# Optimization experiments

Measured on AMD Instinct MI355X. Metric: run time of the kernel, lower is better.

The kernel has to match this reference:

```python
import jax, jax.numpy as jnp
import numpy as np

N_HEADS = 16
D_MODEL = 1024
D_KV = 64


def setup_inputs() -> dict:
    key = jax.random.key(0)
    ks = jax.random.split(key, 5)
    x = jax.random.normal(ks[0], (4, 2048, D_MODEL), dtype=jnp.float32)
    # per-head projections stacked: [H, D_MODEL, D_KV]
    WQ = jax.random.normal(ks[1], (N_HEADS, D_MODEL, D_KV), dtype=jnp.float32) * (D_MODEL ** -0.5)
    WK = jax.random.normal(ks[2], (N_HEADS, D_MODEL, D_KV), dtype=jnp.float32) * (D_MODEL ** -0.5)
    WV = jax.random.normal(ks[3], (N_HEADS, D_MODEL, D_KV), dtype=jnp.float32) * (D_MODEL ** -0.5)
    WO = jax.random.normal(ks[4], (N_HEADS * D_KV, D_MODEL), dtype=jnp.float32) * ((N_HEADS * D_KV) ** -0.5)
    return {"x": x, "WQ": WQ, "WK": WK, "WV": WV, "WO": WO}


def reference(x, WQ, WK, WV, WO):
    # Batched over heads instead of the original per-head Python loop.
    # q,k,v: [B, H, S, Dk]
    q = jnp.einsum('bsd,hdk->bhsk', x, WQ)
    k = jnp.einsum('bsd,hdk->bhsk', x, WK)
    v = jnp.einsum('bsd,hdk->bhsk', x, WV)
    scale = 1.0 / jnp.sqrt(jnp.asarray(q.shape[-1], q.dtype))
    scores = jnp.einsum('bhqk,bhsk->bhqs', q, k) * scale  # [B, H, S, S]
    attn = jax.nn.softmax(scores, axis=-1)
    o = jnp.einsum('bhqs,bhsk->bhqk', attn, v)            # [B, H, S, Dk]
    # concat heads along feature dim == transpose + reshape
    B, H, S, Dk = o.shape
    o = o.transpose(0, 2, 1, 3).reshape(B, S, H * Dk)
    return o @ WO
```

## Files before the change

kernel.cpp:

```cpp
#include <hip/hip_runtime.h>
#include <stdint.h>
#include <stddef.h>


typedef __attribute__((ext_vector_type(8))) short short8;
typedef __attribute__((ext_vector_type(4))) float floatx4;
typedef __attribute__((ext_vector_type(16))) float floatx16;

#define MFMA_BF16(a, b, c) __builtin_amdgcn_mfma_f32_16x16x32_bf16((a), (b), (c), 0, 0, 0)
#define MFMA32_BF16(a, b, c) __builtin_amdgcn_mfma_f32_32x32x16_bf16((a), (b), (c), 0, 0, 0)

__device__ __forceinline__ unsigned short f32_bf16(float f) {
  union { float f; unsigned u; } v; v.f = f;
  unsigned r = v.u + 0x7fffu + ((v.u >> 16) & 1u);
  return (unsigned short)(r >> 16);
}

__device__ __forceinline__ unsigned pack_bf16_rh(float a, float b) {
  unsigned ua = __float_as_uint(a) + 0x8000u;
  unsigned ub = __float_as_uint(b) + 0x8000u;
  return __builtin_amdgcn_perm(ub, ua, 0x07060302u);
}

__device__ __forceinline__ float fast_exp2(float x) {
#if __has_builtin(__builtin_amdgcn_exp2f)
  return __builtin_amdgcn_exp2f(x);
#else
  return exp2f(x);
#endif
}

__device__ __forceinline__ void g2l16(const void* g, void* l) {
  __builtin_amdgcn_global_load_lds((const __attribute__((address_space(1))) void*)g,
                                   (__attribute__((address_space(3))) void*)l,
                                   16, 0, 0);
}


__global__ __launch_bounds__(256) void cvt_x_k(const float* __restrict__ x,
                                               unsigned short* __restrict__ xb) {
  int i = (blockIdx.x * 256 + threadIdx.x) * 4;
  float4 v = *(const float4*)(x + i);
  ushort4 o;
  o.x = f32_bf16(v.x); o.y = f32_bf16(v.y); o.z = f32_bf16(v.z); o.w = f32_bf16(v.w);
  *(ushort4*)(xb + i) = o;
}

__global__ __launch_bounds__(256) void cvt_wqkv_t(const float* __restrict__ WQ,
                                                  const float* __restrict__ WK,
                                                  const float* __restrict__ WV,
                                                  unsigned short* __restrict__ Wt) {
  __shared__ unsigned short tile[64][72];
  const int th = blockIdx.y;
  const int typ = th >> 4, h = th & 15;
  const float* W = (typ == 0) ? WQ : ((typ == 1) ? WK : WV);
  const float* src = W + ((size_t)h * 1024 + blockIdx.x * 64) * 64;
  const int tid = threadIdx.x;
  #pragma unroll
  for (int it = 0; it < 16; ++it) {
    int f = it * 256 + tid;
    int dk = f & 63, dl = f >> 6;
    tile[dk][dl] = f32_bf16(src[(size_t)dl * 64 + dk]);
  }
  __syncthreads();
  unsigned short* dst = Wt + (size_t)(typ * 1024 + h * 64) * 1024 + blockIdx.x * 64;
  #pragma unroll
  for (int it = 0; it < 16; ++it) {
    int f = it * 256 + tid;
    int d = f & 63, dk = f >> 6;
    dst[(size_t)dk * 1024 + d] = tile[dk][d];
  }
}

__global__ __launch_bounds__(256) void cvt_wo_t(const float* __restrict__ WO,
                                                unsigned short* __restrict__ Wt) {
  __shared__ unsigned short tile[64][72];
  const int nt = blockIdx.x * 64, kt = blockIdx.y * 64;
  const int tid = threadIdx.x;
  #pragma unroll
  for (int it = 0; it < 16; ++it) {
    int f = it * 256 + tid;
    int n = f & 63, kl = f >> 6;
    tile[n][kl] = f32_bf16(WO[(size_t)(kt + kl) * 1024 + nt + n]);
  }
  __syncthreads();
  #pragma unroll
  for (int it = 0; it < 16; ++it) {
    int f = it * 256 + tid;
    int k = f & 63, nl = f >> 6;
    Wt[(size_t)(nt + nl) * 1024 + kt + k] = tile[nl][k];
  }
}


__global__ __launch_bounds__(256, 2)
void gemm_qkv_k(const unsigned short* __restrict__ A,
                const unsigned short* __restrict__ Bt,
                unsigned short* __restrict__ Qo,
                unsigned short* __restrict__ Ko,
                unsigned short* __restrict__ Vo) {
  __shared__ __align__(16) unsigned short As[8192];
  __shared__ __align__(16) unsigned short Bs[8192];
  const int lane = threadIdx.x & 63;
  const int wave = threadIdx.x >> 6;
  const int quad = lane >> 4;
  const int t = lane & 15;
  const int wm = wave >> 1, wn = wave & 1;
  const int row0 = blockIdx.y * 128;
  const int col0 = blockIdx.x * 128;

  floatx4 acc[4][4];
  #pragma unroll
  for (int i = 0; i < 4; ++i)
    #pragma unroll
    for (int j = 0; j < 4; ++j) acc[i][j] = (floatx4)0.0f;

  for (int k0 = 0; k0 < 1024; k0 += 64) {
    #pragma unroll
    for (int i = 0; i < 4; ++i) {
      int s = (wave * 4 + i) * 64 + lane;
      int r = s >> 3, kc = (s & 7) ^ (r & 7);
      g2l16(A  + (size_t)(row0 + r) * 1024 + k0 + kc * 8, As + (wave * 4 + i) * 512);
      g2l16(Bt + (size_t)(col0 + r) * 1024 + k0 + kc * 8, Bs + (wave * 4 + i) * 512);
    }
    __syncthreads();
    #pragma unroll
    for (int kk = 0; kk < 2; ++kk) {
      short8 af[4], bf[4];
      #pragma unroll
      for (int mt = 0; mt < 4; ++mt) {
        int r = wm * 64 + mt * 16 + t;
        int kc = (kk * 4 + quad) ^ (r & 7);
        af[mt] = *(const short8*)(As + (r * 8 + kc) * 8);
      }
      #pragma unroll
      for (int nt = 0; nt < 4; ++nt) {
        int r = wn * 64 + nt * 16 + t;
        int kc = (kk * 4 + quad) ^ (r & 7);
        bf[nt] = *(const short8*)(Bs + (r * 8 + kc) * 8);
      }
      #pragma unroll
      for (int mt = 0; mt < 4; ++mt)
        #pragma unroll
        for (int nt = 0; nt < 4; ++nt)
          acc[mt][nt] = MFMA_BF16(af[mt], bf[nt], acc[mt][nt]);
    }
    __syncthreads();
  }

  const int typ = col0 >> 10;
  const float qscale = 0.18033688011112042f;
  const int qp = ((quad & 1) << 1) | (quad >> 1);
  #pragma unroll
  for (int mt = 0; mt < 4; ++mt) {
    int grow0 = row0 + wm * 64 + mt * 16 + quad * 4;
    int b = grow0 >> 11;
    int s = grow0 & 2047;
    #pragma unroll
    for (int nt = 0; nt < 4; ++nt) {
      int gcol = col0 + wn * 64 + nt * 16 + t;
      int rem = gcol & 1023;
      int h = rem >> 6, dk = rem & 63;
      int bhh = b * 16 + h;
      if (typ == 0) {
        #pragma unroll
        for (int rg = 0; rg < 4; ++rg)
          Qo[((size_t)bhh * 2048 + s + rg) * 64 + dk] = f32_bf16(acc[mt][nt][rg] * qscale);
      } else if (typ == 1) {
        #pragma unroll
        for (int rg = 0; rg < 4; ++rg)
          Ko[((size_t)bhh * 2048 + s + rg) * 64 + dk] = f32_bf16(acc[mt][nt][rg]);
      } else {
        ushort4 pv;
        pv.x = f32_bf16(acc[mt][nt][0]);
        pv.y = f32_bf16(acc[mt][nt][1]);
        pv.z = f32_bf16(acc[mt][nt][2]);
        pv.w = f32_bf16(acc[mt][nt][3]);
        int sp = (s & ~15) | (qp << 2);
        *(ushort4*)(Vo + ((size_t)bhh * 64 + dk) * 2048 + sp) = pv;
      }
    }
  }
}


__global__ __launch_bounds__(256, 4)
void attn_k(const unsigned short* __restrict__ Qg_,
            const unsigned short* __restrict__ Kg_,
            const unsigned short* __restrict__ Vg_,
            unsigned short* __restrict__ O) {
  __shared__ __align__(16) char smem[16384];
  const int lane = threadIdx.x & 63;
  const int wave = threadIdx.x >> 6;
  const int h32 = lane >> 5;
  const int c32 = lane & 31;
  const int bh = blockIdx.y;
  const int q0 = blockIdx.x * 128;
  const unsigned short* Qg = Qg_ + ((size_t)bh * 2048 + q0) * 64;
  const unsigned short* Kg = Kg_ + (size_t)bh * 2048 * 64;
  const unsigned short* Vg = Vg_ + (size_t)bh * 64 * 2048;

  short8 qf[4];
  {
    int rq = wave * 32 + c32;
    #pragma unroll
    for (int dc = 0; dc < 4; ++dc)
      qf[dc] = *(const short8*)(Qg + (size_t)rq * 64 + dc * 16 + h32 * 8);
  }

  union { unsigned u[4]; short8 s8; } onesf;
  #pragma unroll
  for (int i = 0; i < 4; ++i) onesf.u[i] = 0x3F803F80u;

  floatx16 acc[2], accs;
  acc[0] = (floatx16)0.0f; acc[1] = (floatx16)0.0f; accs = (floatx16)0.0f;

  for (int s0 = 0; s0 < 2048; s0 += 64) {
    #pragma unroll
    for (int i = 0; i < 2; ++i) {
      int s = (wave * 2 + i) * 64 + lane;
      int r = s >> 3, kc = (s & 7) ^ (r & 7);
      g2l16(Kg + (size_t)(s0 + r) * 64 + kc * 8, smem + (wave * 2 + i) * 1024);
      g2l16(Vg + (size_t)r * 2048 + s0 + kc * 8, smem + 8192 + (wave * 2 + i) * 1024);
    }
    __syncthreads();

    #pragma unroll
    for (int kb = 0; kb < 2; ++kb) {
      floatx16 sc = (floatx16)0.0f;
      #pragma unroll
      for (int dc = 0; dc < 4; ++dc) {
        int rk = kb * 32 + c32;
        int kc = (dc * 2 + h32) ^ (c32 & 7);
        short8 kf = *(const short8*)(smem + (rk * 8 + kc) * 16);
        sc = MFMA32_BF16(kf, qf[dc], sc);
      }
      float p[16];
      #pragma unroll
      for (int r = 0; r < 16; ++r) p[r] = fast_exp2(sc[r]);
      unsigned pk[8];
      #pragma unroll
      for (int i = 0; i < 8; ++i) pk[i] = pack_bf16_rh(p[2 * i], p[2 * i + 1]);
      union { unsigned u[4]; short8 s8; } a0, a1;
      a0.u[0] = pk[0]; a0.u[1] = pk[1]; a0.u[2] = pk[2]; a0.u[3] = pk[3];
      a1.u[0] = pk[4]; a1.u[1] = pk[5]; a1.u[2] = pk[6]; a1.u[3] = pk[7];
      #pragma unroll
      for (int st = 0; st < 2; ++st) {
        short8 af = st ? a1.s8 : a0.s8;
        int cc = kb * 4 + st * 2 + h32;
        #pragma unroll
        for (int nb = 0; nb < 2; ++nb) {
          int rv = nb * 32 + c32;
          short8 bv = *(const short8*)(smem + 8192 + (rv * 8 + (cc ^ (rv & 7))) * 16);
          acc[nb] = MFMA32_BF16(af, bv, acc[nb]);
        }
        accs = MFMA32_BF16(af, onesf.s8, accs);
      }
    }
    __syncthreads();
  }

  const int b = bh >> 4, h = bh & 15;
  #pragma unroll
  for (int g = 0; g < 4; ++g) {
    #pragma unroll
    for (int rr = 0; rr < 4; ++rr) {
      int qrel = rr + 8 * g + 4 * h32;
      float rl = 1.0f / accs[4 * g + rr];
      int token = b * 2048 + q0 + wave * 32 + qrel;
      size_t base = (size_t)token * 1024 + h * 64;
      O[base + c32]      = f32_bf16(acc[0][4 * g + rr] * rl);
      O[base + 32 + c32] = f32_bf16(acc[1][4 * g + rr] * rl);
    }
  }
}


__global__ __launch_bounds__(256, 2)
void gemm_out_k(const unsigned short* __restrict__ A,
                const unsigned short* __restrict__ Bt,
                float* __restrict__ C) {
  __shared__ __align__(16) unsigned short As[8192];
  __shared__ __align__(16) unsigned short Bs[8192];
  const int lane = threadIdx.x & 63;
  const int wave = threadIdx.x >> 6;
  const int quad = lane >> 4;
  const int t = lane & 15;
  const int wm = wave >> 1, wn = wave & 1;
  const int row0 = blockIdx.y * 128;
  const int col0 = blockIdx.x * 128;

  floatx4 acc[4][4];
  #pragma unroll
  for (int i = 0; i < 4; ++i)
    #pragma unroll
    for (int j = 0; j < 4; ++j) acc[i][j] = (floatx4)0.0f;

  for (int k0 = 0; k0 < 1024; k0 += 64) {
    #pragma unroll
    for (int i = 0; i < 4; ++i) {
      int s = (wave * 4 + i) * 64 + lane;
      int r = s >> 3, kc = (s & 7) ^ (r & 7);
      g2l16(A  + (size_t)(row0 + r) * 1024 + k0 + kc * 8, As + (wave * 4 + i) * 512);
      g2l16(Bt + (size_t)(col0 + r) * 1024 + k0 + kc * 8, Bs + (wave * 4 + i) * 512);
    }
    __syncthreads();
    #pragma unroll
    for (int kk = 0; kk < 2; ++kk) {
      short8 af[4], bf[4];
      #pragma unroll
      for (int mt = 0; mt < 4; ++mt) {
        int r = wm * 64 + mt * 16 + t;
        int kc = (kk * 4 + quad) ^ (r & 7);
        af[mt] = *(const short8*)(As + (r * 8 + kc) * 8);
      }
      #pragma unroll
      for (int nt = 0; nt < 4; ++nt) {
        int r = wn * 64 + nt * 16 + t;
        int kc = (kk * 4 + quad) ^ (r & 7);
        bf[nt] = *(const short8*)(Bs + (r * 8 + kc) * 8);
      }
      #pragma unroll
      for (int mt = 0; mt < 4; ++mt)
        #pragma unroll
        for (int nt = 0; nt < 4; ++nt)
          acc[mt][nt] = MFMA_BF16(af[mt], bf[nt], acc[mt][nt]);
    }
    __syncthreads();
  }

  #pragma unroll
  for (int mt = 0; mt < 4; ++mt) {
    int grow0 = row0 + wm * 64 + mt * 16 + quad * 4;
    #pragma unroll
    for (int nt = 0; nt < 4; ++nt) {
      int gcol = col0 + wn * 64 + nt * 16 + t;
      #pragma unroll
      for (int rg = 0; rg < 4; ++rg)
        C[(size_t)(grow0 + rg) * 1024 + gcol] = acc[mt][nt][rg];
    }
  }
}


extern "C" void kernel_launch(void* const* d_in, const int* in_sizes, int n_in,
                              void* d_out, int out_size, void* d_ws, size_t ws_size,
                              hipStream_t stream) {
  const float* x  = (const float*)d_in[0];
  const float* WQ = (const float*)d_in[1];
  const float* WK = (const float*)d_in[2];
  const float* WV = (const float*)d_in[3];
  const float* WO = (const float*)d_in[4];
  char* ws = (char*)d_ws;
  unsigned short* xb   = (unsigned short*)(ws);
  unsigned short* Wqkv = (unsigned short*)(ws + (size_t)16 * 1024 * 1024);
  unsigned short* WOt  = (unsigned short*)(ws + (size_t)22 * 1024 * 1024);
  unsigned short* Qb   = (unsigned short*)(ws + (size_t)24 * 1024 * 1024);
  unsigned short* Kb   = (unsigned short*)(ws + (size_t)40 * 1024 * 1024);
  unsigned short* Vb   = (unsigned short*)(ws + (size_t)56 * 1024 * 1024);
  float* out = (float*)d_out;

  cvt_x_k<<<8192, 256, 0, stream>>>(x, xb);
  cvt_wqkv_t<<<dim3(16, 48), 256, 0, stream>>>(WQ, WK, WV, Wqkv);
  cvt_wo_t<<<dim3(16, 16), 256, 0, stream>>>(WO, WOt);
  gemm_qkv_k<<<dim3(24, 64), 256, 0, stream>>>(xb, Wqkv, Qb, Kb, Vb);
  attn_k<<<dim3(16, 64), 256, 0, stream>>>(Qb, Kb, Vb, xb );
  gemm_out_k<<<dim3(8, 64), 256, 0, stream>>>(xb, WOt, out);
}
```

Baseline: 261.5 us.

## Double per-wave query rows in attention and merge weight conversion kernels

Each attention wave now processes two 32-row query groups against a shared 128-key K/V tile, so every LDS K/V fragment read feeds two MFMAs and the key loop runs half as many iterations with half as many barriers. The block now covers 256 queries, the grid is reordered so head-batch is the fast dimension, LDS doubles to 32KB and the occupancy hint drops to 2 blocks per CU. The two weight transpose-convert kernels are merged into a single launch. The cost is higher register pressure from the doubled accumulators and fewer resident blocks for hiding latency.

```diff
diff --git a/kernel.cpp b/kernel.cpp
--- a/kernel.cpp
+++ b/kernel.cpp
@@ -46,49 +46,50 @@
   *(ushort4*)(xb + i) = o;
 }
 
-__global__ __launch_bounds__(256) void cvt_wqkv_t(const float* __restrict__ WQ,
-                                                  const float* __restrict__ WK,
-                                                  const float* __restrict__ WV,
-                                                  unsigned short* __restrict__ Wt) {
+__global__ __launch_bounds__(256) void cvt_w_k(const float* __restrict__ WQ,
+                                               const float* __restrict__ WK,
+                                               const float* __restrict__ WV,
+                                               const float* __restrict__ WO,
+                                               unsigned short* __restrict__ Wqkv,
+                                               unsigned short* __restrict__ WOt) {
   __shared__ unsigned short tile[64][72];
-  const int th = blockIdx.y;
-  const int typ = th >> 4, h = th & 15;
-  const float* W = (typ == 0) ? WQ : ((typ == 1) ? WK : WV);
-  const float* src = W + ((size_t)h * 1024 + blockIdx.x * 64) * 64;
+  const int bid = blockIdx.x;
   const int tid = threadIdx.x;
-  #pragma unroll
-  for (int it = 0; it < 16; ++it) {
-    int f = it * 256 + tid;
-    int dk = f & 63, dl = f >> 6;
-    tile[dk][dl] = f32_bf16(src[(size_t)dl * 64 + dk]);
-  }
-  __syncthreads();
-  unsigned short* dst = Wt + (size_t)(typ * 1024 + h * 64) * 1024 + blockIdx.x * 64;
-  #pragma unroll
-  for (int it = 0; it < 16; ++it) {
-    int f = it * 256 + tid;
-    int d = f & 63, dk = f >> 6;
-    dst[(size_t)dk * 1024 + d] = tile[dk][d];
-  }
-}
-
-__global__ __launch_bounds__(256) void cvt_wo_t(const float* __restrict__ WO,
-                                                unsigned short* __restrict__ Wt) {
-  __shared__ unsigned short tile[64][72];
-  const int nt = blockIdx.x * 64, kt = blockIdx.y * 64;
-  const int tid = threadIdx.x;
-  #pragma unroll
-  for (int it = 0; it < 16; ++it) {
-    int f = it * 256 + tid;
-    int n = f & 63, kl = f >> 6;
-    tile[n][kl] = f32_bf16(WO[(size_t)(kt + kl) * 1024 + nt + n]);
-  }
-  __syncthreads();
-  #pragma unroll
-  for (int it = 0; it < 16; ++it) {
-    int f = it * 256 + tid;
-    int k = f & 63, nl = f >> 6;
-    Wt[(size_t)(nt + nl) * 1024 + kt + k] = tile[nl][k];
+  if (bid < 768) {
+    const int th = bid >> 4;
+    const int typ = th >> 4, h = th & 15;
+    const float* W = (typ == 0) ? WQ : ((typ == 1) ? WK : WV);
+    const float* src = W + ((size_t)h * 1024 + (bid & 15) * 64) * 64;
+    #pragma unroll
+    for (int it = 0; it < 16; ++it) {
+      int f = it * 256 + tid;
+      int dk = f & 63, dl = f >> 6;
+      tile[dk][dl] = f32_bf16(src[(size_t)dl * 64 + dk]);
+    }
+    __syncthreads();
+    unsigned short* dst = Wqkv + (size_t)(typ * 1024 + h * 64) * 1024 + (bid & 15) * 64;
+    #pragma unroll
+    for (int it = 0; it < 16; ++it) {
+      int f = it * 256 + tid;
+      int d = f & 63, dk = f >> 6;
+      dst[(size_t)dk * 1024 + d] = tile[dk][d];
+    }
+  } else {
+    const int id2 = bid - 768;
+    const int nt = (id2 & 15) * 64, kt = (id2 >> 4) * 64;
+    #pragma unroll
+    for (int it = 0; it < 16; ++it) {
+      int f = it * 256 + tid;
+      int n = f & 63, kl = f >> 6;
+      tile[n][kl] = f32_bf16(WO[(size_t)(kt + kl) * 1024 + nt + n]);
+    }
+    __syncthreads();
+    #pragma unroll
+    for (int it = 0; it < 16; ++it) {
+      int f = it * 256 + tid;
+      int k = f & 63, nl = f >> 6;
+      WOt[(size_t)(nt + nl) * 1024 + kt + k] = tile[nl][k];
+    }
   }
 }
 
@@ -184,77 +185,86 @@
 }
 
 
-__global__ __launch_bounds__(256, 4)
+__global__ __launch_bounds__(256, 2)
 void attn_k(const unsigned short* __restrict__ Qg_,
             const unsigned short* __restrict__ Kg_,
             const unsigned short* __restrict__ Vg_,
             unsigned short* __restrict__ O) {
-  __shared__ __align__(16) char smem[16384];
+  __shared__ __align__(16) char smem[32768];
   const int lane = threadIdx.x & 63;
   const int wave = threadIdx.x >> 6;
   const int h32 = lane >> 5;
   const int c32 = lane & 31;
-  const int bh = blockIdx.y;
-  const int q0 = blockIdx.x * 128;
+  const int bh = blockIdx.x;
+  const int q0 = blockIdx.y * 256;
   const unsigned short* Qg = Qg_ + ((size_t)bh * 2048 + q0) * 64;
   const unsigned short* Kg = Kg_ + (size_t)bh * 2048 * 64;
   const unsigned short* Vg = Vg_ + (size_t)bh * 64 * 2048;
 
-  short8 qf[4];
-  {
-    int rq = wave * 32 + c32;
+  short8 qf[2][4];
+  #pragma unroll
+  for (int g = 0; g < 2; ++g) {
+    int rq = wave * 64 + g * 32 + c32;
     #pragma unroll
     for (int dc = 0; dc < 4; ++dc)
-      qf[dc] = *(const short8*)(Qg + (size_t)rq * 64 + dc * 16 + h32 * 8);
+      qf[g][dc] = *(const short8*)(Qg + (size_t)rq * 64 + dc * 16 + h32 * 8);
   }
 
   union { unsigned u[4]; short8 s8; } onesf;
   #pragma unroll
   for (int i = 0; i < 4; ++i) onesf.u[i] = 0x3F803F80u;
 
-  floatx16 acc[2], accs;
-  acc[0] = (floatx16)0.0f; acc[1] = (floatx16)0.0f; accs = (floatx16)0.0f;
-
-  for (int s0 = 0; s0 < 2048; s0 += 64) {
-    #pragma unroll
-    for (int i = 0; i < 2; ++i) {
-      int s = (wave * 2 + i) * 64 + lane;
-      int r = s >> 3, kc = (s & 7) ^ (r & 7);
-      g2l16(Kg + (size_t)(s0 + r) * 64 + kc * 8, smem + (wave * 2 + i) * 1024);
-      g2l16(Vg + (size_t)r * 2048 + s0 + kc * 8, smem + 8192 + (wave * 2 + i) * 1024);
-    }
-    __syncthreads();
-
-    #pragma unroll
-    for (int kb = 0; kb < 2; ++kb) {
-      floatx16 sc = (floatx16)0.0f;
+  floatx16 acc[2][2], accs[2];
+  #pragma unroll
+  for (int g = 0; g < 2; ++g) {
+    acc[g][0] = (floatx16)0.0f; acc[g][1] = (floatx16)0.0f; accs[g] = (floatx16)0.0f;
+  }
+
+  for (int s0 = 0; s0 < 2048; s0 += 128) {
+    #pragma unroll
+    for (int i = 0; i < 4; ++i) {
+      int s = (wave * 4 + i) * 64 + lane;
+      int rk = s >> 3, ck = (s & 7) ^ (rk & 7);
+      g2l16(Kg + (size_t)(s0 + rk) * 64 + ck * 8, smem + s * 16);
+      int rv = s >> 4, cv = (s & 15) ^ (rv & 7);
+      g2l16(Vg + (size_t)rv * 2048 + s0 + cv * 8, smem + 16384 + s * 16);
+    }
+    __syncthreads();
+
+    #pragma unroll
+    for (int kb = 0; kb < 4; ++kb) {
+      floatx16 sc0 = (floatx16)0.0f, sc1 = (floatx16)0.0f;
       #pragma unroll
       for (int dc = 0; dc < 4; ++dc) {
         int rk = kb * 32 + c32;
-        int kc = (dc * 2 + h32) ^ (c32 & 7);
+        int kc = (dc * 2 + h32) ^ (rk & 7);
         short8 kf = *(const short8*)(smem + (rk * 8 + kc) * 16);
-        sc = MFMA32_BF16(kf, qf[dc], sc);
-      }
-      float p[16];
-      #pragma unroll
-      for (int r = 0; r < 16; ++r) p[r] = fast_exp2(sc[r]);
-      unsigned pk[8];
-      #pragma unroll
-      for (int i = 0; i < 8; ++i) pk[i] = pack_bf16_rh(p[2 * i], p[2 * i + 1]);
-      union { unsigned u[4]; short8 s8; } a0, a1;
-      a0.u[0] = pk[0]; a0.u[1] = pk[1]; a0.u[2] = pk[2]; a0.u[3] = pk[3];
-      a1.u[0] = pk[4]; a1.u[1] = pk[5]; a1.u[2] = pk[6]; a1.u[3] = pk[7];
+        sc0 = MFMA32_BF16(kf, qf[0][dc], sc0);
+        sc1 = MFMA32_BF16(kf, qf[1][dc], sc1);
+      }
+      unsigned pk0[8], pk1[8];
+      #pragma unroll
+      for (int i = 0; i < 8; ++i) {
+        float a0 = fast_exp2(sc0[2 * i]), b0 = fast_exp2(sc0[2 * i + 1]);
+        float a1 = fast_exp2(sc1[2 * i]), b1 = fast_exp2(sc1[2 * i + 1]);
+        pk0[i] = pack_bf16_rh(a0, b0);
+        pk1[i] = pack_bf16_rh(a1, b1);
+      }
       #pragma unroll
       for (int st = 0; st < 2; ++st) {
-        short8 af = st ? a1.s8 : a0.s8;
+        union { unsigned u[4]; short8 s8; } af0, af1;
+        #pragma unroll
+        for (int i = 0; i < 4; ++i) { af0.u[i] = pk0[4 * st + i]; af1.u[i] = pk1[4 * st + i]; }
         int cc = kb * 4 + st * 2 + h32;
         #pragma unroll
         for (int nb = 0; nb < 2; ++nb) {
           int rv = nb * 32 + c32;
-          short8 bv = *(const short8*)(smem + 8192 + (rv * 8 + (cc ^ (rv & 7))) * 16);
-          acc[nb] = MFMA32_BF16(af, bv, acc[nb]);
+          short8 bv = *(const short8*)(smem + 16384 + (rv * 16 + (cc ^ (rv & 7))) * 16);
+          acc[0][nb] = MFMA32_BF16(af0.s8, bv, acc[0][nb]);
+          acc[1][nb] = MFMA32_BF16(af1.s8, bv, acc[1][nb]);
         }
-        accs = MFMA32_BF16(af, onesf.s8, accs);
+        accs[0] = MFMA32_BF16(af0.s8, onesf.s8, accs[0]);
+        accs[1] = MFMA32_BF16(af1.s8, onesf.s8, accs[1]);
       }
     }
     __syncthreads();
@@ -262,15 +272,18 @@
 
   const int b = bh >> 4, h = bh & 15;
   #pragma unroll
-  for (int g = 0; g < 4; ++g) {
-    #pragma unroll
-    for (int rr = 0; rr < 4; ++rr) {
-      int qrel = rr + 8 * g + 4 * h32;
-      float rl = 1.0f / accs[4 * g + rr];
-      int token = b * 2048 + q0 + wave * 32 + qrel;
-      size_t base = (size_t)token * 1024 + h * 64;
-      O[base + c32]      = f32_bf16(acc[0][4 * g + rr] * rl);
-      O[base + 32 + c32] = f32_bf16(acc[1][4 * g + rr] * rl);
+  for (int g = 0; g < 2; ++g) {
+    #pragma unroll
+    for (int gg = 0; gg < 4; ++gg) {
+      #pragma unroll
+      for (int rr = 0; rr < 4; ++rr) {
+        int qrel = rr + 8 * gg + 4 * h32;
+        float rl = 1.0f / accs[g][4 * gg + rr];
+        int token = b * 2048 + q0 + wave * 64 + g * 32 + qrel;
+        size_t base = (size_t)token * 1024 + h * 64;
+        O[base + c32]      = f32_bf16(acc[g][0][4 * gg + rr] * rl);
+        O[base + 32 + c32] = f32_bf16(acc[g][1][4 * gg + rr] * rl);
+      }
     }
   }
 }
@@ -361,9 +374,8 @@
   float* out = (float*)d_out;
 
   cvt_x_k<<<8192, 256, 0, stream>>>(x, xb);
-  cvt_wqkv_t<<<dim3(16, 48), 256, 0, stream>>>(WQ, WK, WV, Wqkv);
-  cvt_wo_t<<<dim3(16, 16), 256, 0, stream>>>(WO, WOt);
+  cvt_w_k<<<1024, 256, 0, stream>>>(WQ, WK, WV, WO, Wqkv, WOt);
   gemm_qkv_k<<<dim3(24, 64), 256, 0, stream>>>(xb, Wqkv, Qb, Kb, Vb);
-  attn_k<<<dim3(16, 64), 256, 0, stream>>>(Qb, Kb, Vb, xb );
+  attn_k<<<dim3(64, 8), 256, 0, stream>>>(Qb, Kb, Vb, xb );
   gemm_out_k<<<dim3(8, 64), 256, 0, stream>>>(xb, WOt, out);
 }
```

Result: faster. 250.9 us (-4.1%).
